# Kernel optimization log

Measured on AMD Instinct MI355X. Metric: run time of the kernel, lower is better.

The kernel has to match this reference:

```python
import jax, jax.numpy as jnp
import numpy as np

B, F, N, H = 512, 2, 128, 256
CAR_LOAD = 20.0


def setup_inputs() -> dict:
    key = jax.random.key(0)
    ks = jax.random.split(key, 12)
    rnd = lambda k, shape: (jax.random.normal(k, shape) * 0.05).astype(jnp.float32)
    return {
        'static': jax.random.uniform(ks[0], (B, F, N), dtype=jnp.float32),
        'dynamic': jax.random.uniform(ks[1], (B, F, N), dtype=jnp.float32, minval=0.1, maxval=1.0),
        'last_hh': jnp.zeros((B, H), dtype=jnp.float32),
        'Ws': rnd(ks[2], (H, F)), 'bs': jnp.zeros((H,), jnp.float32),
        'Wd': rnd(ks[3], (H, F)), 'bd': jnp.zeros((H,), jnp.float32),
        'Wdec': rnd(ks[4], (H, F)), 'bdec': jnp.zeros((H,), jnp.float32),
        'W_ih': rnd(ks[5], (3 * H, H)), 'W_hh': rnd(ks[6], (3 * H, H)),
        'b_ih': jnp.zeros((3 * H,), jnp.float32), 'b_hh': jnp.zeros((3 * H,), jnp.float32),
        'Wa': rnd(ks[7], (H, 3 * H)), 'va': rnd(ks[8], (H,)),
        'Wp': rnd(ks[9], (H, 2 * H)), 'vp': rnd(ks[10], (H,)),
    }


def reference(static, dynamic, last_hh, Ws, bs, Wd, bd, Wdec, bdec,
              W_ih, W_hh, b_ih, b_hh, Wa, va, Wp, vp):
    Bn, Fn, Nn = static.shape
    Hn = Ws.shape[0]
    # update_fn is None -> dynamic is constant except the load channel, which the
    # loop overwrites with car_load every step before encoding.
    dyn = dynamic.at[:, 0, :].set(CAR_LOAD)
    # 1x1 Conv1d encoders == per-node linear maps
    static_h = jnp.einsum('hf,bfn->bhn', Ws, static) + bs[None, :, None]   # [B,H,N]
    dyn_h = jnp.einsum('hf,bfn->bhn', Wd, dyn) + bd[None, :, None]          # [B,H,N]
    # Attention W acts on cat(static_h, dyn_h, rnn_out); split into blocks and
    # precompute the step-invariant (static+dynamic) part once.
    Wa_s, Wa_d, Wa_h = Wa[:, :Hn], Wa[:, Hn:2 * Hn], Wa[:, 2 * Hn:]
    pre_attn = (jnp.einsum('hk,bkn->bhn', Wa_s, static_h)
                + jnp.einsum('hk,bkn->bhn', Wa_d, dyn_h))                   # [B,H,N]
    Wp_s, Wp_c = Wp[:, :Hn], Wp[:, Hn:]
    pre_ptr = jnp.einsum('hk,bkn->bhn', Wp_s, static_h)                     # [B,H,N]

    def gru_step(x, h):  # torch nn.GRU single layer, batch_first, seq_len=1
        gi = x @ W_ih.T + b_ih
        gh = h @ W_hh.T + b_hh
        ir, iz, inn = jnp.split(gi, 3, axis=-1)
        hr, hz, hn = jnp.split(gh, 3, axis=-1)
        r = jax.nn.sigmoid(ir + hr)
        z = jax.nn.sigmoid(iz + hz)
        n = jnp.tanh(inn + r * hn)
        return (1.0 - z) * n + z * h

    def step(carry, _):
        idx, h = carry
        # decoder_input = gather of static coords at current tour position
        dec_in = jnp.take_along_axis(static, idx[:, None, None], axis=2)[:, :, 0]  # [B,F]
        dec_h = dec_in @ Wdec.T + bdec                                             # [B,H]
        h = gru_step(dec_h, h)
        # Bahdanau-style tanh attention: v . tanh(W [static; dyn; rnn_out])
        u = jnp.tanh(pre_attn + (h @ Wa_h.T)[:, :, None])                          # [B,H,N]
        attn = jax.nn.softmax(jnp.einsum('h,bhn->bn', va, u), axis=1)
        context = jnp.einsum('bn,bhn->bh', attn, static_h)                         # [B,H]
        e = jnp.tanh(pre_ptr + (context @ Wp_c.T)[:, :, None])                     # [B,H,N]
        logits = jnp.einsum('h,bhn->bn', vp, e)
        # mask_fn is None -> mask all ones -> log(mask)=0
        probs = jax.nn.softmax(logits, axis=1)
        ptr = jnp.argmax(probs, axis=1).astype(jnp.int32)  # eval-mode greedy decode
        logp = jnp.log(jnp.max(probs, axis=1))
        return (ptr, h), (ptr, logp)

    idx0 = jnp.zeros((Bn,), dtype=jnp.int32)  # tour starts at depot 0
    _, (tour_idx, tour_logp) = jax.lax.scan(step, (idx0, last_hh), None, length=Nn)
    return tour_idx.T, tour_logp.T  # [B, N] each
```

## Files before the change

kernel.cpp:

```cpp
#include <hip/hip_runtime.h>
#include <math.h>


#define NB 512
#define NF 2
#define NN 128
#define NH 256
#define NH3 768
#define SC 2.8853900817779268f

typedef float v2f __attribute__((ext_vector_type(2)));

__device__ __forceinline__ float fast_rcp(float x) { return __builtin_amdgcn_rcpf(x); }
__device__ __forceinline__ float fast_exp2(float x) { return __builtin_amdgcn_exp2f(x); }
__device__ __forceinline__ float sigm(float x) { return fast_rcp(1.0f + __expf(-x)); }
__device__ __forceinline__ float tanh_raw(float x) { return 1.0f - 2.0f * fast_rcp(1.0f + fast_exp2(SC * x)); }
__device__ __forceinline__ v2f vsplat(float a) { v2f r; r.x = a; r.y = a; return r; }
__device__ __forceinline__ v2f vfma(v2f a, v2f b, v2f c) { return __builtin_elementwise_fma(a, b, c); }


__global__ void precompute_kernel(const float* __restrict__ Ws, const float* __restrict__ bs,
                                  const float* __restrict__ Wd, const float* __restrict__ bd,
                                  const float* __restrict__ Wdec, const float* __restrict__ bdec,
                                  const float* __restrict__ W_ih, const float* __restrict__ b_ih,
                                  const float* __restrict__ Wa, const float* __restrict__ va,
                                  const float* __restrict__ Wp, const float* __restrict__ vp,
                                  float* __restrict__ ws)
{
    int tid = blockIdx.x * blockDim.x + threadIdx.x;
    if (tid < 768) {
        int j = tid; const float* wr = &W_ih[j * NH];
        float m0 = 0.f, m1 = 0.f;
        for (int k = 0; k < NH; k++) { float w = wr[k]; m0 = fmaf(w, Wdec[2*k], m0); m1 = fmaf(w, Wdec[2*k+1], m1); }
        ws[2*j] = m0; ws[2*j+1] = m1;
    } else if (tid < 1536) {
        int j = tid - 768; const float* wr = &W_ih[j * NH];
        float c = b_ih[j];
        for (int k = 0; k < NH; k++) c = fmaf(wr[k], bdec[k], c);
        ws[1536 + j] = c;
    } else if (tid < 1792) {
        int h = tid - 1536; const float* war = &Wa[h * NH3];
        float as0 = 0.f, as1 = 0.f, ad1 = 0.f;
        for (int k = 0; k < NH; k++) {
            float w = war[k];
            as0 = fmaf(w, Ws[2*k], as0); as1 = fmaf(w, Ws[2*k+1], as1);
            ad1 = fmaf(war[NH + k], Wd[2*k+1], ad1);
        }
        float4 v = make_float4(SC*as0, SC*as1, SC*ad1, -2.0f*va[h]);
        ((float4*)(ws + 2304))[h] = v;
    } else if (tid < 2048) {
        int h = tid - 1792; const float* war = &Wa[h * NH3];
        float a = 0.f;
        for (int k = 0; k < NH; k++) {
            a = fmaf(war[k], bs[k], a);
            a = fmaf(war[NH + k], fmaf(20.0f, Wd[2*k], bd[k]), a);
        }
        ws[3328 + h] = SC * a;
    } else if (tid < 2304) {
        int h = tid - 2048; const float* wpr = &Wp[h * 2 * NH];
        float p0 = 0.f, p1 = 0.f;
        for (int k = 0; k < NH; k++) { float w = wpr[k]; p0 = fmaf(w, Ws[2*k], p0); p1 = fmaf(w, Ws[2*k+1], p1); }
        float4 v = make_float4(SC*p0, SC*p1, -2.0f*vp[h], 0.f);
        ((float4*)(ws + 3584))[h] = v;
    } else if (tid < 2560) {
        int h = tid - 2304;
        const float* wps = &Wp[h * 2 * NH];
        const float* wpc = wps + NH;
        float p0 = 0.f, p1 = 0.f, pb = 0.f;
        for (int k = 0; k < NH; k++) {
            p0 = fmaf(wpc[k], Ws[2*k], p0);
            p1 = fmaf(wpc[k], Ws[2*k+1], p1);
            pb = fmaf(wps[k] + wpc[k], bs[k], pb);
        }
        float4 v = make_float4(SC*p0, SC*p1, SC*pb, 0.f);
        ((float4*)(ws + 70912))[h] = v;
    } else if (tid < 2560 + 65536) {
        int m = tid - 2560; int i = m >> 8, j = m & 255;
        ws[5376 + m] = SC * Wa[i * NH3 + 2 * NH + j];
    }
}

__global__ void __launch_bounds__(1024, 4)
drl_main(const float* __restrict__ gstatic, const float* __restrict__ gdyn,
         const float* __restrict__ glast, const float* __restrict__ gWhh,
         const float* __restrict__ gbhh, const float* __restrict__ wsb,
         float* __restrict__ out)
{
    __shared__ float s0[2][NN], s1[2][NN], d1[2][NN];
    __shared__ v2f hs2[NH];
    __shared__ float ghs[2][NH3];
    __shared__ float qp[2][NH];
    __shared__ float4 cA[NH];
    __shared__ float4 cP[NH];
    __shared__ float4 cP2[NH];
    __shared__ float2 Mgi[NH3];
    __shared__ float cgi[NH3], bhh[NH3];
    __shared__ float a0v[NH];
    __shared__ float spart[2][NN * 20];
    __shared__ float Sw[2][2];
    __shared__ int idxs[2];

    const int t = threadIdx.x;
    const int g = t >> 9;
    const int r = t & 511;
    const int b0 = blockIdx.x * 2;

    for (int i = t; i < 2 * NN; i += 1024) {
        int gg = i >> 7, n = i & 127, b = b0 + gg;
        s0[gg][n] = gstatic[b * (NF * NN) + n];
        s1[gg][n] = gstatic[b * (NF * NN) + NN + n];
        d1[gg][n] = gdyn[b * (NF * NN) + NN + n];
    }
    for (int i = t; i < 2 * NH; i += 1024) {
        int gg = i >> 8, j = i & 255;
        ((float*)hs2)[2 * j + gg] = glast[(b0 + gg) * NH + j];
    }
    for (int i = t; i < 1536; i += 1024) ((float*)Mgi)[i] = wsb[i];
    if (t < 768) cgi[t] = wsb[1536 + t];
    if (t < 1024) ((float*)cA)[t] = wsb[2304 + t];
    if (t < 256) a0v[t] = wsb[3328 + t];
    if (t < 1024) ((float*)cP)[t] = wsb[3584 + t];
    if (t < 1024) ((float*)cP2)[t] = wsb[70912 + t];
    if (t < 768) bhh[t] = gbhh[t];
    if (t == 0) { idxs[0] = 0; idxs[1] = 0; }
    __syncthreads();

    const float* WaH = wsb + 5376;
    const int jb = t >> 3, kq = t & 7;
    const int jb2 = t >> 2, kh = t & 3;

    const int ng = r >> 4, hg = r & 15;
    const int n0 = ng * 4;
    v2f sa0, sa1, da, sb0, sb1, db;
    sa0.x = s0[g][n0];     sa0.y = s0[g][n0 + 1];
    sa1.x = s1[g][n0];     sa1.y = s1[g][n0 + 1];
    da.x  = d1[g][n0];     da.y  = d1[g][n0 + 1];
    sb0.x = s0[g][n0 + 2]; sb0.y = s0[g][n0 + 3];
    sb1.x = s1[g][n0 + 2]; sb1.y = s1[g][n0 + 3];
    db.x  = d1[g][n0 + 2]; db.y  = d1[g][n0 + 3];
    float cwsum, vpsum;
    {
        float cw = 0.f, vq = 0.f;
        #pragma unroll 8
        for (int hl = 0; hl < 16; hl++) {
            cw += cA[hg + 16 * hl].w;
            vq += cP[hg + 16 * hl].z;
        }
        cwsum = -0.5f * cw; vpsum = -0.5f * vq;
    }

    {
        v2f acc[6];
        #pragma unroll
        for (int i = 0; i < 6; i++) { acc[i].x = 0.f; acc[i].y = 0.f; }
        const float* wb = gWhh + jb * NH + 4 * kq;
        #pragma unroll 2
        for (int c = 0; c < 8; c++) {
            float4 p01 = *(const float4*)&((float*)hs2)[2 * (32 * c + 4 * kq)];
            float4 p23 = *(const float4*)&((float*)hs2)[2 * (32 * c + 4 * kq) + 4];
            v2f hk0, hk1, hk2, hk3;
            hk0.x = p01.x; hk0.y = p01.y; hk1.x = p01.z; hk1.y = p01.w;
            hk2.x = p23.x; hk2.y = p23.y; hk3.x = p23.z; hk3.y = p23.w;
            #pragma unroll
            for (int p = 0; p < 6; p++) {
                float4 w = *(const float4*)(wb + p * 128 * NH + 32 * c);
                acc[p] = vfma(vsplat(w.x), hk0, vfma(vsplat(w.y), hk1,
                         vfma(vsplat(w.z), hk2, vfma(vsplat(w.w), hk3, acc[p]))));
            }
        }
        #pragma unroll
        for (int p = 0; p < 6; p++) {
            float u0 = acc[p].x, u1 = acc[p].y;
            u0 += __shfl_xor(u0, 1); u0 += __shfl_xor(u0, 2); u0 += __shfl_xor(u0, 4);
            u1 += __shfl_xor(u1, 1); u1 += __shfl_xor(u1, 2); u1 += __shfl_xor(u1, 4);
            if (kq == 0) { int j = jb + 128 * p; ghs[0][j] = u0 + bhh[j]; ghs[1][j] = u1 + bhh[j]; }
        }
    }
    __syncthreads();

    for (int step = 0; step < NN; step++) {
        if (r < 256) {
            int id = idxs[g];
            float svA = s0[g][id], svB = s1[g][id];
            float2 m0 = Mgi[r], m1 = Mgi[NH + r], m2 = Mgi[2 * NH + r];
            float ir  = fmaf(m0.x, svA, fmaf(m0.y, svB, cgi[r]));
            float iz  = fmaf(m1.x, svA, fmaf(m1.y, svB, cgi[NH + r]));
            float inn = fmaf(m2.x, svA, fmaf(m2.y, svB, cgi[2 * NH + r]));
            float rr = sigm(ir + ghs[g][r]);
            float zz = sigm(iz + ghs[g][NH + r]);
            float nv = tanh_raw(fmaf(rr, ghs[g][2 * NH + r], inn));
            float ho = ((float*)hs2)[2 * r + g];
            ((float*)hs2)[2 * r + g] = fmaf(zz, ho - nv, nv);
        }
        __syncthreads();
        {
            v2f u; u.x = 0.f; u.y = 0.f;
            const float* wq = WaH + jb2 * NH + 4 * kh;
            #pragma unroll 4
            for (int ks = 0; ks < 16; ks++) {
                float4 w  = *(const float4*)(wq + ks * 16);
                float4 p01 = *(const float4*)&((float*)hs2)[2 * (ks * 16 + 4 * kh)];
                float4 p23 = *(const float4*)&((float*)hs2)[2 * (ks * 16 + 4 * kh) + 4];
                v2f hk0, hk1, hk2, hk3;
                hk0.x = p01.x; hk0.y = p01.y; hk1.x = p01.z; hk1.y = p01.w;
                hk2.x = p23.x; hk2.y = p23.y; hk3.x = p23.z; hk3.y = p23.w;
                u = vfma(vsplat(w.x), hk0, vfma(vsplat(w.y), hk1,
                    vfma(vsplat(w.z), hk2, vfma(vsplat(w.w), hk3, u))));
            }
            u.x += __shfl_xor(u.x, 1); u.x += __shfl_xor(u.x, 2);
            u.y += __shfl_xor(u.y, 1); u.y += __shfl_xor(u.y, 2);
            if (kh == 0) { qp[0][jb2] = u.x + a0v[jb2]; qp[1][jb2] = u.y + a0v[jb2]; }
        }
        __syncthreads();
        {
            v2f at_a = vsplat(cwsum), at_b = vsplat(cwsum);
            v2f g0, g1, g2;
            g0.x = 0.f; g0.y = 0.f; g1.x = 0.f; g1.y = 0.f; g2.x = 0.f; g2.y = 0.f;
            const float* wb = gWhh + jb * NH + 4 * kq;
            #pragma unroll 1
            for (int ks = 0; ks < 8; ks++) {
                float4 w0 = *(const float4*)(wb + 0 * 128 * NH + ks * 32);
                float4 w1 = *(const float4*)(wb + 1 * 128 * NH + ks * 32);
                float4 w2 = *(const float4*)(wb + 2 * 128 * NH + ks * 32);
                #pragma unroll
                for (int u = 0; u < 2; u++) {
                    int h = hg + 16 * (2 * ks + u);
                    float4 c4 = cA[h];
                    float qv = qp[g][h];
                    v2f xa = vfma(vsplat(c4.x), sa0, vfma(vsplat(c4.y), sa1,
                             vfma(vsplat(c4.z), da, vsplat(qv))));
                    v2f xb = vfma(vsplat(c4.x), sb0, vfma(vsplat(c4.y), sb1,
                             vfma(vsplat(c4.z), db, vsplat(qv))));
                    v2f ea, eb;
                    ea.x = fast_exp2(xa.x); ea.y = fast_exp2(xa.y);
                    eb.x = fast_exp2(xb.x); eb.y = fast_exp2(xb.y);
                    v2f ta = ea + 1.0f, tb = eb + 1.0f;
                    float pa = ta.x * ta.y, pb = tb.x * tb.y;
                    float rd = fast_rcp(pa * pb);
                    float m = c4.w * rd;
                    at_a = vfma(vsplat(m * pb), ta.yx, at_a);
                    at_b = vfma(vsplat(m * pa), tb.yx, at_b);
                }
                float4 p01 = *(const float4*)&((float*)hs2)[2 * (ks * 32 + 4 * kq)];
                float4 p23 = *(const float4*)&((float*)hs2)[2 * (ks * 32 + 4 * kq) + 4];
                v2f hk0, hk1, hk2, hk3;
                hk0.x = p01.x; hk0.y = p01.y; hk1.x = p01.z; hk1.y = p01.w;
                hk2.x = p23.x; hk2.y = p23.y; hk3.x = p23.z; hk3.y = p23.w;
                g0 = vfma(vsplat(w0.x), hk0, vfma(vsplat(w0.y), hk1,
                     vfma(vsplat(w0.z), hk2, vfma(vsplat(w0.w), hk3, g0))));
                g1 = vfma(vsplat(w1.x), hk0, vfma(vsplat(w1.y), hk1,
                     vfma(vsplat(w1.z), hk2, vfma(vsplat(w1.w), hk3, g1))));
                g2 = vfma(vsplat(w2.x), hk0, vfma(vsplat(w2.y), hk1,
                     vfma(vsplat(w2.z), hk2, vfma(vsplat(w2.w), hk3, g2))));
            }
            spart[g][(n0 + 0) * 20 + hg] = at_a.x;
            spart[g][(n0 + 1) * 20 + hg] = at_a.y;
            spart[g][(n0 + 2) * 20 + hg] = at_b.x;
            spart[g][(n0 + 3) * 20 + hg] = at_b.y;
            g0.x += __shfl_xor(g0.x, 1); g0.x += __shfl_xor(g0.x, 2); g0.x += __shfl_xor(g0.x, 4);
            g0.y += __shfl_xor(g0.y, 1); g0.y += __shfl_xor(g0.y, 2); g0.y += __shfl_xor(g0.y, 4);
            g1.x += __shfl_xor(g1.x, 1); g1.x += __shfl_xor(g1.x, 2); g1.x += __shfl_xor(g1.x, 4);
            g1.y += __shfl_xor(g1.y, 1); g1.y += __shfl_xor(g1.y, 2); g1.y += __shfl_xor(g1.y, 4);
            g2.x += __shfl_xor(g2.x, 1); g2.x += __shfl_xor(g2.x, 2); g2.x += __shfl_xor(g2.x, 4);
            g2.y += __shfl_xor(g2.y, 1); g2.y += __shfl_xor(g2.y, 2); g2.y += __shfl_xor(g2.y, 4);
            if (kq == 0) {
                ghs[0][jb]       = g0.x + bhh[jb];
                ghs[1][jb]       = g0.y + bhh[jb];
                ghs[0][jb + 128] = g1.x + bhh[jb + 128];
                ghs[1][jb + 128] = g1.y + bhh[jb + 128];
                ghs[0][jb + 256] = g2.x + bhh[jb + 256];
                ghs[1][jb + 256] = g2.y + bhh[jb + 256];
            }
        }
        __syncthreads();
        if (r < 64) {
            int l = r;
            const float* sp0 = &spart[g][l * 20];
            const float* sp1 = &spart[g][(l + 64) * 20];
            float4 q0 = *(const float4*)(sp0), q1 = *(const float4*)(sp0 + 4);
            float4 q2 = *(const float4*)(sp0 + 8), q3 = *(const float4*)(sp0 + 12);
            float v0 = ((q0.x+q0.y)+(q0.z+q0.w)) + ((q1.x+q1.y)+(q1.z+q1.w))
                     + ((q2.x+q2.y)+(q2.z+q2.w)) + ((q3.x+q3.y)+(q3.z+q3.w));
            q0 = *(const float4*)(sp1); q1 = *(const float4*)(sp1 + 4);
            q2 = *(const float4*)(sp1 + 8); q3 = *(const float4*)(sp1 + 12);
            float v1 = ((q0.x+q0.y)+(q0.z+q0.w)) + ((q1.x+q1.y)+(q1.z+q1.w))
                     + ((q2.x+q2.y)+(q2.z+q2.w)) + ((q3.x+q3.y)+(q3.z+q3.w));
            float m = fmaxf(v0, v1);
            #pragma unroll
            for (int o = 32; o; o >>= 1) m = fmaxf(m, __shfl_xor(m, o));
            float e0 = __expf(v0 - m), e1 = __expf(v1 - m);
            float ss = e0 + e1;
            #pragma unroll
            for (int o = 32; o; o >>= 1) ss += __shfl_xor(ss, o);
            float rs = fast_rcp(ss);
            float w0 = e0 * rs, w1 = e1 * rs;
            float t0 = fmaf(w0, s0[g][l], w1 * s0[g][l + 64]);
            float t1 = fmaf(w0, s1[g][l], w1 * s1[g][l + 64]);
            #pragma unroll
            for (int o = 32; o; o >>= 1) { t0 += __shfl_xor(t0, o); t1 += __shfl_xor(t1, o); }
            if (l == 0) { Sw[g][0] = t0; Sw[g][1] = t1; }
        }
        __syncthreads();
        {
            float S0 = Sw[g][0], S1 = Sw[g][1];
            v2f at_a = vsplat(vpsum), at_b = vsplat(vpsum);
            v2f g0, g1, g2;
            g0.x = 0.f; g0.y = 0.f; g1.x = 0.f; g1.y = 0.f; g2.x = 0.f; g2.y = 0.f;
            const float* wb = gWhh + (384 + jb) * NH + 4 * kq;
            #pragma unroll 1
            for (int ks = 0; ks < 8; ks++) {
                float4 w0 = *(const float4*)(wb + 0 * 128 * NH + ks * 32);
                float4 w1 = *(const float4*)(wb + 1 * 128 * NH + ks * 32);
                float4 w2 = *(const float4*)(wb + 2 * 128 * NH + ks * 32);
                #pragma unroll
                for (int u = 0; u < 2; u++) {
                    int h = hg + 16 * (2 * ks + u);
                    float4 c4 = cP[h];
                    float4 c2 = cP2[h];
                    float pc = fmaf(c2.x, S0, fmaf(c2.y, S1, c2.z));
                    v2f xa = vfma(vsplat(c4.x), sa0, vfma(vsplat(c4.y), sa1, vsplat(pc)));
                    v2f xb = vfma(vsplat(c4.x), sb0, vfma(vsplat(c4.y), sb1, vsplat(pc)));
                    v2f ea, eb;
                    ea.x = fast_exp2(xa.x); ea.y = fast_exp2(xa.y);
                    eb.x = fast_exp2(xb.x); eb.y = fast_exp2(xb.y);
                    v2f ta = ea + 1.0f, tb = eb + 1.0f;
                    float pa = ta.x * ta.y, pb = tb.x * tb.y;
                    float rd = fast_rcp(pa * pb);
                    float m = c4.z * rd;
                    at_a = vfma(vsplat(m * pb), ta.yx, at_a);
                    at_b = vfma(vsplat(m * pa), tb.yx, at_b);
                }
                float4 p01 = *(const float4*)&((float*)hs2)[2 * (ks * 32 + 4 * kq)];
                float4 p23 = *(const float4*)&((float*)hs2)[2 * (ks * 32 + 4 * kq) + 4];
                v2f hk0, hk1, hk2, hk3;
                hk0.x = p01.x; hk0.y = p01.y; hk1.x = p01.z; hk1.y = p01.w;
                hk2.x = p23.x; hk2.y = p23.y; hk3.x = p23.z; hk3.y = p23.w;
                g0 = vfma(vsplat(w0.x), hk0, vfma(vsplat(w0.y), hk1,
                     vfma(vsplat(w0.z), hk2, vfma(vsplat(w0.w), hk3, g0))));
                g1 = vfma(vsplat(w1.x), hk0, vfma(vsplat(w1.y), hk1,
                     vfma(vsplat(w1.z), hk2, vfma(vsplat(w1.w), hk3, g1))));
                g2 = vfma(vsplat(w2.x), hk0, vfma(vsplat(w2.y), hk1,
                     vfma(vsplat(w2.z), hk2, vfma(vsplat(w2.w), hk3, g2))));
            }
            spart[g][(n0 + 0) * 20 + hg] = at_a.x;
            spart[g][(n0 + 1) * 20 + hg] = at_a.y;
            spart[g][(n0 + 2) * 20 + hg] = at_b.x;
            spart[g][(n0 + 3) * 20 + hg] = at_b.y;
            g0.x += __shfl_xor(g0.x, 1); g0.x += __shfl_xor(g0.x, 2); g0.x += __shfl_xor(g0.x, 4);
            g0.y += __shfl_xor(g0.y, 1); g0.y += __shfl_xor(g0.y, 2); g0.y += __shfl_xor(g0.y, 4);
            g1.x += __shfl_xor(g1.x, 1); g1.x += __shfl_xor(g1.x, 2); g1.x += __shfl_xor(g1.x, 4);
            g1.y += __shfl_xor(g1.y, 1); g1.y += __shfl_xor(g1.y, 2); g1.y += __shfl_xor(g1.y, 4);
            g2.x += __shfl_xor(g2.x, 1); g2.x += __shfl_xor(g2.x, 2); g2.x += __shfl_xor(g2.x, 4);
            g2.y += __shfl_xor(g2.y, 1); g2.y += __shfl_xor(g2.y, 2); g2.y += __shfl_xor(g2.y, 4);
            if (kq == 0) {
                ghs[0][384 + jb] = g0.x + bhh[384 + jb];
                ghs[1][384 + jb] = g0.y + bhh[384 + jb];
                ghs[0][512 + jb] = g1.x + bhh[512 + jb];
                ghs[1][512 + jb] = g1.y + bhh[512 + jb];
                ghs[0][640 + jb] = g2.x + bhh[640 + jb];
                ghs[1][640 + jb] = g2.y + bhh[640 + jb];
            }
        }
        __syncthreads();
        if (r < 64) {
            int l = r;
            const float* sp0 = &spart[g][l * 20];
            const float* sp1 = &spart[g][(l + 64) * 20];
            float4 q0 = *(const float4*)(sp0), q1 = *(const float4*)(sp0 + 4);
            float4 q2 = *(const float4*)(sp0 + 8), q3 = *(const float4*)(sp0 + 12);
            float v0 = ((q0.x+q0.y)+(q0.z+q0.w)) + ((q1.x+q1.y)+(q1.z+q1.w))
                     + ((q2.x+q2.y)+(q2.z+q2.w)) + ((q3.x+q3.y)+(q3.z+q3.w));
            q0 = *(const float4*)(sp1); q1 = *(const float4*)(sp1 + 4);
            q2 = *(const float4*)(sp1 + 8); q3 = *(const float4*)(sp1 + 12);
            float v1 = ((q0.x+q0.y)+(q0.z+q0.w)) + ((q1.x+q1.y)+(q1.z+q1.w))
                     + ((q2.x+q2.y)+(q2.z+q2.w)) + ((q3.x+q3.y)+(q3.z+q3.w));
            float bv = v0; int bi = l;
            if (v1 > v0) { bv = v1; bi = l + 64; }
            #pragma unroll
            for (int o = 32; o; o >>= 1) {
                float ov = __shfl_xor(bv, o); int oi = __shfl_xor(bi, o);
                if (ov > bv || (ov == bv && oi < bi)) { bv = ov; bi = oi; }
            }
            float e0 = __expf(v0 - bv), e1 = __expf(v1 - bv);
            float ss = e0 + e1;
            #pragma unroll
            for (int o = 32; o; o >>= 1) ss += __shfl_xor(ss, o);
            if (l == 0) {
                idxs[g] = bi;
                int b = b0 + g;
                out[b * NN + step] = (float)bi;
                out[NB * NN + b * NN + step] = -logf(ss);
            }
        }
        __syncthreads();
    }
}

extern "C" void kernel_launch(void* const* d_in, const int* in_sizes, int n_in,
                              void* d_out, int out_size, void* d_ws, size_t ws_size,
                              hipStream_t stream) {
    const float* gstatic = (const float*)d_in[0];
    const float* gdyn    = (const float*)d_in[1];
    const float* glast   = (const float*)d_in[2];
    const float* Ws      = (const float*)d_in[3];
    const float* bs      = (const float*)d_in[4];
    const float* Wd      = (const float*)d_in[5];
    const float* bd      = (const float*)d_in[6];
    const float* Wdec    = (const float*)d_in[7];
    const float* bdec    = (const float*)d_in[8];
    const float* W_ih    = (const float*)d_in[9];
    const float* W_hh    = (const float*)d_in[10];
    const float* b_ih    = (const float*)d_in[11];
    const float* b_hh    = (const float*)d_in[12];
    const float* Wa      = (const float*)d_in[13];
    const float* va      = (const float*)d_in[14];
    const float* Wp      = (const float*)d_in[15];
    const float* vp      = (const float*)d_in[16];
    float* outp = (float*)d_out;
    float* wsb  = (float*)d_ws;

    precompute_kernel<<<267, 256, 0, stream>>>(Ws, bs, Wd, bd, Wdec, bdec,
                                               W_ih, b_ih, Wa, va, Wp, vp, wsb);
    drl_main<<<256, 1024, 0, stream>>>(gstatic, gdyn, glast, W_hh, b_hh, wsb, outp);
}
```

Measured before the change: 2.076 ms.

## Reduce GRU partials via LDS and drop max-subtraction in softmax reductions

The per-lane shuffle reductions of the hidden-state gate partials are replaced with stores to a new shared buffer. Otherwise-idle threads (64..447) then reduce that buffer in the same phase as the attention/pointer softmax work, so the two overlap behind one barrier. The softmax paths drop the separate max-reduction pass. Attention sums exp-weighted values and normalises once at the end, and the pointer path folds the sum-exp into the argmax shuffle loop. The risk is exp overflow or precision loss without max subtraction, plus extra LDS traffic and footprint.

```diff
diff --git a/kernel.cpp b/kernel.cpp
--- a/kernel.cpp
+++ b/kernel.cpp
@@ -97,6 +97,7 @@
     __shared__ float cgi[NH3], bhh[NH3];
     __shared__ float a0v[NH];
     __shared__ float spart[2][NN * 20];
+    __shared__ float gpart[384 * 20];
     __shared__ float Sw[2][2];
     __shared__ int idxs[2];
 
@@ -257,48 +258,51 @@
             spart[g][(n0 + 1) * 20 + hg] = at_a.y;
             spart[g][(n0 + 2) * 20 + hg] = at_b.x;
             spart[g][(n0 + 3) * 20 + hg] = at_b.y;
-            g0.x += __shfl_xor(g0.x, 1); g0.x += __shfl_xor(g0.x, 2); g0.x += __shfl_xor(g0.x, 4);
-            g0.y += __shfl_xor(g0.y, 1); g0.y += __shfl_xor(g0.y, 2); g0.y += __shfl_xor(g0.y, 4);
-            g1.x += __shfl_xor(g1.x, 1); g1.x += __shfl_xor(g1.x, 2); g1.x += __shfl_xor(g1.x, 4);
-            g1.y += __shfl_xor(g1.y, 1); g1.y += __shfl_xor(g1.y, 2); g1.y += __shfl_xor(g1.y, 4);
-            g2.x += __shfl_xor(g2.x, 1); g2.x += __shfl_xor(g2.x, 2); g2.x += __shfl_xor(g2.x, 4);
-            g2.y += __shfl_xor(g2.y, 1); g2.y += __shfl_xor(g2.y, 2); g2.y += __shfl_xor(g2.y, 4);
-            if (kq == 0) {
-                ghs[0][jb]       = g0.x + bhh[jb];
-                ghs[1][jb]       = g0.y + bhh[jb];
-                ghs[0][jb + 128] = g1.x + bhh[jb + 128];
-                ghs[1][jb + 128] = g1.y + bhh[jb + 128];
-                ghs[0][jb + 256] = g2.x + bhh[jb + 256];
-                ghs[1][jb + 256] = g2.y + bhh[jb + 256];
-            }
-        }
-        __syncthreads();
-        if (r < 64) {
-            int l = r;
-            const float* sp0 = &spart[g][l * 20];
-            const float* sp1 = &spart[g][(l + 64) * 20];
-            float4 q0 = *(const float4*)(sp0), q1 = *(const float4*)(sp0 + 4);
-            float4 q2 = *(const float4*)(sp0 + 8), q3 = *(const float4*)(sp0 + 12);
-            float v0 = ((q0.x+q0.y)+(q0.z+q0.w)) + ((q1.x+q1.y)+(q1.z+q1.w))
-                     + ((q2.x+q2.y)+(q2.z+q2.w)) + ((q3.x+q3.y)+(q3.z+q3.w));
-            q0 = *(const float4*)(sp1); q1 = *(const float4*)(sp1 + 4);
-            q2 = *(const float4*)(sp1 + 8); q3 = *(const float4*)(sp1 + 12);
-            float v1 = ((q0.x+q0.y)+(q0.z+q0.w)) + ((q1.x+q1.y)+(q1.z+q1.w))
-                     + ((q2.x+q2.y)+(q2.z+q2.w)) + ((q3.x+q3.y)+(q3.z+q3.w));
-            float m = fmaxf(v0, v1);
-            #pragma unroll
-            for (int o = 32; o; o >>= 1) m = fmaxf(m, __shfl_xor(m, o));
-            float e0 = __expf(v0 - m), e1 = __expf(v1 - m);
-            float ss = e0 + e1;
-            #pragma unroll
-            for (int o = 32; o; o >>= 1) ss += __shfl_xor(ss, o);
-            float rs = fast_rcp(ss);
-            float w0 = e0 * rs, w1 = e1 * rs;
-            float t0 = fmaf(w0, s0[g][l], w1 * s0[g][l + 64]);
-            float t1 = fmaf(w0, s1[g][l], w1 * s1[g][l + 64]);
-            #pragma unroll
-            for (int o = 32; o; o >>= 1) { t0 += __shfl_xor(t0, o); t1 += __shfl_xor(t1, o); }
-            if (l == 0) { Sw[g][0] = t0; Sw[g][1] = t1; }
+            *(v2f*)&gpart[(jb      ) * 20 + (kq << 1)] = g0;
+            *(v2f*)&gpart[(jb + 128) * 20 + (kq << 1)] = g1;
+            *(v2f*)&gpart[(jb + 256) * 20 + (kq << 1)] = g2;
+        }
+        __syncthreads();
+        {
+            int v = t - 64;
+            if (t >= 64 && v < 384) {
+                const float* gp = &gpart[v * 20];
+                float4 q0 = *(const float4*)(gp);
+                float4 q1 = *(const float4*)(gp + 4);
+                float4 q2 = *(const float4*)(gp + 8);
+                float4 q3 = *(const float4*)(gp + 12);
+                float sg0 = ((q0.x + q0.z) + (q1.x + q1.z)) + ((q2.x + q2.z) + (q3.x + q3.z));
+                float sg1 = ((q0.y + q0.w) + (q1.y + q1.w)) + ((q2.y + q2.w) + (q3.y + q3.w));
+                ghs[0][v] = sg0 + bhh[v];
+                ghs[1][v] = sg1 + bhh[v];
+            }
+            if (r < 64) {
+                int l = r;
+                const float* sp0 = &spart[g][l * 20];
+                const float* sp1 = &spart[g][(l + 64) * 20];
+                float4 q0 = *(const float4*)(sp0), q1 = *(const float4*)(sp0 + 4);
+                float4 q2 = *(const float4*)(sp0 + 8), q3 = *(const float4*)(sp0 + 12);
+                float v0 = ((q0.x+q0.y)+(q0.z+q0.w)) + ((q1.x+q1.y)+(q1.z+q1.w))
+                         + ((q2.x+q2.y)+(q2.z+q2.w)) + ((q3.x+q3.y)+(q3.z+q3.w));
+                q0 = *(const float4*)(sp1); q1 = *(const float4*)(sp1 + 4);
+                q2 = *(const float4*)(sp1 + 8); q3 = *(const float4*)(sp1 + 12);
+                float v1 = ((q0.x+q0.y)+(q0.z+q0.w)) + ((q1.x+q1.y)+(q1.z+q1.w))
+                         + ((q2.x+q2.y)+(q2.z+q2.w)) + ((q3.x+q3.y)+(q3.z+q3.w));
+                float e0 = __expf(v0), e1 = __expf(v1);
+                float aa = e0 + e1;
+                float bb = fmaf(e0, s0[g][l], e1 * s0[g][l + 64]);
+                float cc = fmaf(e0, s1[g][l], e1 * s1[g][l + 64]);
+                #pragma unroll
+                for (int o = 32; o; o >>= 1) {
+                    aa += __shfl_xor(aa, o);
+                    bb += __shfl_xor(bb, o);
+                    cc += __shfl_xor(cc, o);
+                }
+                if (l == 0) {
+                    float rs = fast_rcp(aa);
+                    Sw[g][0] = bb * rs; Sw[g][1] = cc * rs;
+                }
+            }
         }
         __syncthreads();
         {
@@ -346,50 +350,51 @@
             spart[g][(n0 + 1) * 20 + hg] = at_a.y;
             spart[g][(n0 + 2) * 20 + hg] = at_b.x;
             spart[g][(n0 + 3) * 20 + hg] = at_b.y;
-            g0.x += __shfl_xor(g0.x, 1); g0.x += __shfl_xor(g0.x, 2); g0.x += __shfl_xor(g0.x, 4);
-            g0.y += __shfl_xor(g0.y, 1); g0.y += __shfl_xor(g0.y, 2); g0.y += __shfl_xor(g0.y, 4);
-            g1.x += __shfl_xor(g1.x, 1); g1.x += __shfl_xor(g1.x, 2); g1.x += __shfl_xor(g1.x, 4);
-            g1.y += __shfl_xor(g1.y, 1); g1.y += __shfl_xor(g1.y, 2); g1.y += __shfl_xor(g1.y, 4);
-            g2.x += __shfl_xor(g2.x, 1); g2.x += __shfl_xor(g2.x, 2); g2.x += __shfl_xor(g2.x, 4);
-            g2.y += __shfl_xor(g2.y, 1); g2.y += __shfl_xor(g2.y, 2); g2.y += __shfl_xor(g2.y, 4);
-            if (kq == 0) {
-                ghs[0][384 + jb] = g0.x + bhh[384 + jb];
-                ghs[1][384 + jb] = g0.y + bhh[384 + jb];
-                ghs[0][512 + jb] = g1.x + bhh[512 + jb];
-                ghs[1][512 + jb] = g1.y + bhh[512 + jb];
-                ghs[0][640 + jb] = g2.x + bhh[640 + jb];
-                ghs[1][640 + jb] = g2.y + bhh[640 + jb];
-            }
-        }
-        __syncthreads();
-        if (r < 64) {
-            int l = r;
-            const float* sp0 = &spart[g][l * 20];
-            const float* sp1 = &spart[g][(l + 64) * 20];
-            float4 q0 = *(const float4*)(sp0), q1 = *(const float4*)(sp0 + 4);
-            float4 q2 = *(const float4*)(sp0 + 8), q3 = *(const float4*)(sp0 + 12);
-            float v0 = ((q0.x+q0.y)+(q0.z+q0.w)) + ((q1.x+q1.y)+(q1.z+q1.w))
-                     + ((q2.x+q2.y)+(q2.z+q2.w)) + ((q3.x+q3.y)+(q3.z+q3.w));
-            q0 = *(const float4*)(sp1); q1 = *(const float4*)(sp1 + 4);
-            q2 = *(const float4*)(sp1 + 8); q3 = *(const float4*)(sp1 + 12);
-            float v1 = ((q0.x+q0.y)+(q0.z+q0.w)) + ((q1.x+q1.y)+(q1.z+q1.w))
-                     + ((q2.x+q2.y)+(q2.z+q2.w)) + ((q3.x+q3.y)+(q3.z+q3.w));
-            float bv = v0; int bi = l;
-            if (v1 > v0) { bv = v1; bi = l + 64; }
-            #pragma unroll
-            for (int o = 32; o; o >>= 1) {
-                float ov = __shfl_xor(bv, o); int oi = __shfl_xor(bi, o);
-                if (ov > bv || (ov == bv && oi < bi)) { bv = ov; bi = oi; }
-            }
-            float e0 = __expf(v0 - bv), e1 = __expf(v1 - bv);
-            float ss = e0 + e1;
-            #pragma unroll
-            for (int o = 32; o; o >>= 1) ss += __shfl_xor(ss, o);
-            if (l == 0) {
-                idxs[g] = bi;
-                int b = b0 + g;
-                out[b * NN + step] = (float)bi;
-                out[NB * NN + b * NN + step] = -logf(ss);
+            *(v2f*)&gpart[(jb      ) * 20 + (kq << 1)] = g0;
+            *(v2f*)&gpart[(jb + 128) * 20 + (kq << 1)] = g1;
+            *(v2f*)&gpart[(jb + 256) * 20 + (kq << 1)] = g2;
+        }
+        __syncthreads();
+        {
+            int v = t - 64;
+            if (t >= 64 && v < 384) {
+                const float* gp = &gpart[v * 20];
+                float4 q0 = *(const float4*)(gp);
+                float4 q1 = *(const float4*)(gp + 4);
+                float4 q2 = *(const float4*)(gp + 8);
+                float4 q3 = *(const float4*)(gp + 12);
+                float sg0 = ((q0.x + q0.z) + (q1.x + q1.z)) + ((q2.x + q2.z) + (q3.x + q3.z));
+                float sg1 = ((q0.y + q0.w) + (q1.y + q1.w)) + ((q2.y + q2.w) + (q3.y + q3.w));
+                ghs[0][384 + v] = sg0 + bhh[384 + v];
+                ghs[1][384 + v] = sg1 + bhh[384 + v];
+            }
+            if (r < 64) {
+                int l = r;
+                const float* sp0 = &spart[g][l * 20];
+                const float* sp1 = &spart[g][(l + 64) * 20];
+                float4 q0 = *(const float4*)(sp0), q1 = *(const float4*)(sp0 + 4);
+                float4 q2 = *(const float4*)(sp0 + 8), q3 = *(const float4*)(sp0 + 12);
+                float v0 = ((q0.x+q0.y)+(q0.z+q0.w)) + ((q1.x+q1.y)+(q1.z+q1.w))
+                         + ((q2.x+q2.y)+(q2.z+q2.w)) + ((q3.x+q3.y)+(q3.z+q3.w));
+                q0 = *(const float4*)(sp1); q1 = *(const float4*)(sp1 + 4);
+                q2 = *(const float4*)(sp1 + 8); q3 = *(const float4*)(sp1 + 12);
+                float v1 = ((q0.x+q0.y)+(q0.z+q0.w)) + ((q1.x+q1.y)+(q1.z+q1.w))
+                         + ((q2.x+q2.y)+(q2.z+q2.w)) + ((q3.x+q3.y)+(q3.z+q3.w));
+                float bv = v0; int bi = l;
+                if (v1 > v0) { bv = v1; bi = l + 64; }
+                float es = __expf(v0) + __expf(v1);
+                #pragma unroll
+                for (int o = 32; o; o >>= 1) {
+                    float ov = __shfl_xor(bv, o); int oi = __shfl_xor(bi, o);
+                    es += __shfl_xor(es, o);
+                    if (ov > bv || (ov == bv && oi < bi)) { bv = ov; bi = oi; }
+                }
+                if (l == 0) {
+                    idxs[g] = bi;
+                    int b = b0 + g;
+                    out[b * NN + step] = (float)bi;
+                    out[NB * NN + b * NN + step] = bv - logf(es);
+                }
             }
         }
         __syncthreads();
```

New measurement: 1.965 ms. 1.06x faster.
